# Kernel optimization log

Hardware: AMD Instinct MI355X
Metric: run time of the kernel (lower is better)

Reference implementation:

```python
import jax, jax.numpy as jnp
import numpy as np

ROPE_BASE = 10000.0
CHUNK = 2048
NEG_INF = -1e30


def _rope(q, k, start_index):
    # q, k: (B, T, H, Dh) with Dh even; half-split RoPE as in RotaryEmbedding
    B, T, H, Dh = q.shape
    half = Dh // 2
    inv_freq = jnp.exp(jnp.arange(half, dtype=jnp.float32) * (-(np.log(ROPE_BASE) / half)))
    pos = jnp.arange(T, dtype=jnp.float32) + jnp.float32(start_index)
    ang = pos[:, None] * inv_freq[None, :]              # (T, half)
    cos = jnp.cos(ang)[None, :, None, :].astype(q.dtype)  # (1,T,1,half)
    sin = jnp.sin(ang)[None, :, None, :].astype(q.dtype)

    def rot(x):
        x1, x2 = x[..., :half], x[..., half:]
        return jnp.concatenate([x1 * cos - x2 * sin, x2 * cos + x1 * sin], axis=-1)

    return rot(q), rot(k)


def reference(q, k, v, start_index):
    # Chunked causal self-attention, softmax(QK^T) V with scale = 1.0 (Megalodon Eq. 9).
    B, T, H, Dh = q.shape
    Dv = v.shape[-1]
    q, k = _rope(q, k, start_index)

    nc = T // CHUNK  # T assumed multiple of chunk_size (prefill path, no cache)
    qc = q.reshape(B, nc, CHUNK, H, Dh)
    kc = k.reshape(B, nc, CHUNK, H, Dh)
    vc = v.reshape(B, nc, CHUNK, H, Dv)

    # per-chunk causal mask (C, C): 0 where j <= i else -inf
    i = jnp.arange(CHUNK)
    causal = (i[None, :] <= i[:, None])

    scores = jnp.einsum('bnqhd,bnkhd->bnhqk', qc, kc)  # scale = 1.0
    scores = jnp.where(causal[None, None, None, :, :], scores, NEG_INF)
    probs = jax.nn.softmax(scores, axis=-1)
    out = jnp.einsum('bnhqk,bnkhd->bnqhd', probs, vc)
    return out.reshape(B, T, H, Dv)


def setup_inputs() -> dict:
    key = jax.random.key(0)
    kq, kk, kv = jax.random.split(key, 3)
    B, T, H, Dh, Dv = 2, 4096, 16, 128, 128
    return {
        'q': jax.random.normal(kq, (B, T, H, Dh), dtype=jnp.float32),
        'k': jax.random.normal(kk, (B, T, H, Dh), dtype=jnp.float32),
        'v': jax.random.normal(kv, (B, T, H, Dv), dtype=jnp.float32),
        'start_index': 0,
    }
```

## Files before the change

### kernel.cpp

```cpp
#include <hip/hip_runtime.h>


#define T_TOT  4096
#define HH     16
#define DH     128
#define CHUNKL 2048
#define QT     128
#define KTILE  64
#define THREADS 256
#define NEGV   1e30f
#define L2E    1.44269504088896f
#define THRL2  11.5415603f

typedef _Float16 f16;
typedef __attribute__((ext_vector_type(8)))  _Float16 f16x8;
typedef __attribute__((ext_vector_type(4)))  _Float16 f16x4;
typedef __attribute__((ext_vector_type(2)))  _Float16 f16x2;
typedef __attribute__((ext_vector_type(4)))  float    f32x4;
typedef __attribute__((ext_vector_type(16))) float    f32x16;
typedef __attribute__((ext_vector_type(4)))  int      i32x4;

#define AS_G(p) ((const __attribute__((address_space(1))) void*)(p))
#define AS_L(p) ((__attribute__((address_space(3))) void*)(p))

__device__ __forceinline__ f32x16 mfma32(f16x8 a, f16x8 b, f32x16 c) {
    return __builtin_amdgcn_mfma_f32_32x32x16_f16(a, b, c, 0, 0, 0);
}
__device__ __forceinline__ f32x4 mfma16(f16x8 a, f16x8 b, f32x4 c) {
    return __builtin_amdgcn_mfma_f32_16x16x32_f16(a, b, c, 0, 0, 0);
}
__device__ __forceinline__ int pk2(float a, float b) {
    f16x2 t; t[0] = (f16)a; t[1] = (f16)b;
    return __builtin_bit_cast(int, t);
}

__global__ void rope_table_kernel(float* __restrict__ tab, const int* __restrict__ startp) {
    int gid = blockIdx.x * blockDim.x + threadIdx.x;
    int t = gid >> 6, d = gid & 63;
    float pos  = (float)(t + *startp);
    float invf = expf((float)d * (-9.210340371976184f / 64.0f));
    float s, c;
    sincosf(pos * invf, &s, &c);
    tab[gid] = c;
    tab[T_TOT * 64 + gid] = s;
}

__global__ void prep_kv_kernel(const float* __restrict__ K, const float* __restrict__ V,
                               const float* __restrict__ tab,
                               f16* __restrict__ Kws, f16* __restrict__ VTws) {
    const int half = (2 * T_TOT * HH * DH) / 8;
    int gid = blockIdx.x * blockDim.x + threadIdx.x;
    if (gid < half) {
        const int tile = gid >> 10, idx = gid & 1023;
        const int key = idx >> 4, c8 = idx & 15;
        const int dsw0 = c8 << 3;
        const int sw   = (key & 7) << 3;
        const int d0   = dsw0 ^ sw;
        const int kt = tile & 31, h = (tile >> 5) & 15, n = (tile >> 9) & 1, b = tile >> 10;
        const int t  = n * CHUNKL + kt * KTILE + key;
        const float* kp = K + ((size_t)(b * T_TOT + t) * HH + h) * DH;
        const int dl = d0 & 63;
        f32x4 xm0 = *(const f32x4*)(kp + d0);
        f32x4 xm1 = *(const f32x4*)(kp + d0 + 4);
        f32x4 xo0 = *(const f32x4*)(kp + (d0 ^ 64));
        f32x4 xo1 = *(const f32x4*)(kp + (d0 ^ 64) + 4);
        f32x4 cc0 = *(const f32x4*)(tab + t * 64 + dl);
        f32x4 cc1 = *(const f32x4*)(tab + t * 64 + dl + 4);
        f32x4 ss0 = *(const f32x4*)(tab + T_TOT * 64 + t * 64 + dl);
        f32x4 ss1 = *(const f32x4*)(tab + T_TOT * 64 + t * 64 + dl + 4);
        const float sgn = (d0 < 64) ? -1.f : 1.f;
        f16x8 out;
#pragma unroll
        for (int j = 0; j < 4; ++j) {
            out[j]     = (f16)(xm0[j] * cc0[j] + sgn * xo0[j] * ss0[j]);
            out[4 + j] = (f16)(xm1[j] * cc1[j] + sgn * xo1[j] * ss1[j]);
        }
        *(f16x8*)&Kws[(size_t)tile * 8192 + key * DH + dsw0] = out;
    } else {
        const int oc = gid - half;
        const int tile = oc >> 10, idx = oc & 1023;
        const int d = idx >> 3, c8 = idx & 7;
        const int ksw0 = c8 << 3;
        const int sw   = (d & 7) << 3;
        const int key0 = ksw0 ^ sw;
        const int kt = tile & 31, h = (tile >> 5) & 15, n = (tile >> 9) & 1, b = tile >> 10;
        const int t0 = n * CHUNKL + kt * KTILE + key0;
        const float* vp = V + ((size_t)(b * T_TOT + t0) * HH + h) * DH + d;
        f16x8 out;
#pragma unroll
        for (int j = 0; j < 8; ++j)
            out[j] = (f16)vp[(size_t)j * (HH * DH)];
        *(f16x8*)&VTws[(size_t)tile * 8192 + d * KTILE + ksw0] = out;
    }
}

__global__ __launch_bounds__(THREADS, 2)
void attn_fast_kernel(const float* __restrict__ Q, const f16* __restrict__ Kws,
                      const f16* __restrict__ VTws, const float* __restrict__ tab,
                      float* __restrict__ O)
{
    __shared__ f16 Kl[2][KTILE * DH];
    __shared__ f16 VTl[2][KTILE * DH];

    const int bid = blockIdx.x;
    const int sb  = (bid & 7) * 128 + (bid >> 3);
    const int qt  = 15 - (sb & 15);
    const int bnh = sb >> 4;
    const int hd = bnh & 15, n = (bnh >> 4) & 1, b = bnh >> 5;

    const int tid = threadIdx.x;
    const int w   = tid >> 6;
    const int l   = tid & 63;
    const int hl  = l >> 5;
    const int c31 = l & 31;

    const int q0 = qt * QT;
    const size_t bh = (size_t)b * T_TOT * (HH * DH) + (size_t)hd * DH;
    const size_t tile0 = ((size_t)(((b * 2 + n) * 16 + hd) * 32)) * 8192;

    const int qr = q0 + w * 32 + c31;
    const int tg = n * CHUNKL + qr;
    const float* qp = Q + bh + (size_t)tg * (HH * DH);

    f16x8 qf[8];
#pragma unroll
    for (int ks = 0; ks < 8; ++ks) {
        const int dbase = ks * 16 + 8 * hl;
        const int dl    = dbase & 63;
        f32x4 xa0 = *(const f32x4*)(qp + dbase);
        f32x4 xa1 = *(const f32x4*)(qp + dbase + 4);
        f32x4 xb0 = *(const f32x4*)(qp + (dbase ^ 64));
        f32x4 xb1 = *(const f32x4*)(qp + (dbase ^ 64) + 4);
        float cc[8], ss[8];
        *(f32x4*)&cc[0] = *(const f32x4*)(tab + tg * 64 + dl);
        *(f32x4*)&cc[4] = *(const f32x4*)(tab + tg * 64 + dl + 4);
        *(f32x4*)&ss[0] = *(const f32x4*)(tab + T_TOT * 64 + tg * 64 + dl);
        *(f32x4*)&ss[4] = *(const f32x4*)(tab + T_TOT * 64 + tg * 64 + dl + 4);
        const float sgn = (dbase < 64) ? -1.f : 1.f;
        float xa[8] = {xa0[0],xa0[1],xa0[2],xa0[3],xa1[0],xa1[1],xa1[2],xa1[3]};
        float xb[8] = {xb0[0],xb0[1],xb0[2],xb0[3],xb1[0],xb1[1],xb1[2],xb1[3]};
        f16x8 f;
#pragma unroll
        for (int j = 0; j < 8; ++j)
            f[j] = (f16)((xa[j] * cc[j] + sgn * xb[j] * ss[j]) * L2E);
        qf[ks] = f;
    }

    f32x16 o[4];
    float mrun = -NEGV, lrun = 0.f;
#pragma unroll
    for (int dt = 0; dt < 4; ++dt)
#pragma unroll
        for (int r = 0; r < 16; ++r) o[dt][r] = 0.f;

    const int nkt = 2 * qt + 2;
    int cur = 0;

#pragma unroll
    for (int i = 0; i < 4; ++i) {
        const int off = (i * 4 + w) * 512;
        __builtin_amdgcn_global_load_lds(AS_G(Kws  + tile0 + off + l * 8), AS_L(&Kl[0][off]),  16, 0, 0);
        __builtin_amdgcn_global_load_lds(AS_G(VTws + tile0 + off + l * 8), AS_L(&VTl[0][off]), 16, 0, 0);
    }

    for (int kt = 0; kt < nkt; ++kt) {
        __syncthreads();

        if (kt + 1 < nkt) {
            const f16* ks_ = Kws  + tile0 + (size_t)(kt + 1) * 8192;
            const f16* vs_ = VTws + tile0 + (size_t)(kt + 1) * 8192;
            const int nb = cur ^ 1;
#pragma unroll
            for (int i = 0; i < 4; ++i) {
                const int off = (i * 4 + w) * 512;
                __builtin_amdgcn_global_load_lds(AS_G(ks_ + off + l * 8), AS_L(&Kl[nb][off]),  16, 0, 0);
                __builtin_amdgcn_global_load_lds(AS_G(vs_ + off + l * 8), AS_L(&VTl[nb][off]), 16, 0, 0);
            }
        }

        const bool active = (kt * KTILE) < (q0 + w * 32 + 32);
        if (active) {
            const f16* Klc  = Kl[cur];
            const f16* VTlc = VTl[cur];

            f32x16 s[2];
#pragma unroll
            for (int ts = 0; ts < 2; ++ts)
#pragma unroll
                for (int r = 0; r < 16; ++r) s[ts][r] = 0.f;

            __builtin_amdgcn_s_setprio(1);
#pragma unroll
            for (int ts = 0; ts < 2; ++ts) {
                const int key = ts * 32 + c31;
                const int swk = (key & 7) << 3;
#pragma unroll
                for (int ks = 0; ks < 8; ++ks) {
                    f16x8 kf = *(const f16x8*)&Klc[key * DH + ((ks * 16 + 8 * hl) ^ swk)];
                    s[ts] = mfma32(kf, qf[ks], s[ts]);
                }
            }
            __builtin_amdgcn_s_setprio(0);

            if (kt >= 2 * qt) {
#pragma unroll
                for (int ts = 0; ts < 2; ++ts)
#pragma unroll
                    for (int r = 0; r < 16; ++r) {
                        const int key = kt * KTILE + ts * 32 + (r & 3) + 8 * (r >> 2) + 4 * hl;
                        if (key > qr) s[ts][r] = -NEGV;
                    }
            }

            float mx = s[0][0];
#pragma unroll
            for (int r = 1; r < 16; ++r) mx = fmaxf(mx, s[0][r]);
#pragma unroll
            for (int r = 0; r < 16; ++r) mx = fmaxf(mx, s[1][r]);
            mx = fmaxf(mx, __shfl_xor(mx, 32));

            if (__any(mx > mrun + THRL2)) {
                const float mn = fmaxf(mrun, mx);
                const float al = exp2f(mrun - mn);
                mrun = mn;
                lrun *= al;
#pragma unroll
                for (int dt = 0; dt < 4; ++dt)
#pragma unroll
                    for (int r = 0; r < 16; ++r) o[dt][r] *= al;
            }

            float ps = 0.f;
#pragma unroll
            for (int ts = 0; ts < 2; ++ts)
#pragma unroll
                for (int r = 0; r < 16; ++r) {
                    const float p = exp2f(s[ts][r] - mrun);
                    s[ts][r] = p;
                    ps += p;
                }
            lrun += ps;

            f16x8 pb[4];
#pragma unroll
            for (int ts = 0; ts < 2; ++ts) {
#pragma unroll
                for (int gs = 0; gs < 2; ++gs) {
                    const int G = 8 * gs;
                    const int A  = pk2(s[ts][G + 0], s[ts][G + 1]);
                    const int Bw = pk2(s[ts][G + 2], s[ts][G + 3]);
                    const int C  = pk2(s[ts][G + 4], s[ts][G + 5]);
                    const int Dw = pk2(s[ts][G + 6], s[ts][G + 7]);
                    const int Y1 = hl ? A : C;
                    const int Y2 = hl ? Bw : Dw;
                    const int r1 = __shfl_xor(Y1, 32);
                    const int r2 = __shfl_xor(Y2, 32);
                    i32x4 bi;
                    bi[0] = hl ? r1 : A;
                    bi[1] = hl ? r2 : Bw;
                    bi[2] = hl ? C  : r1;
                    bi[3] = hl ? Dw : r2;
                    pb[2 * ts + gs] = __builtin_bit_cast(f16x8, bi);
                }
            }

            __builtin_amdgcn_s_setprio(1);
#pragma unroll
            for (int dt = 0; dt < 4; ++dt) {
                const int d   = dt * 32 + c31;
                const int swv = (d & 7) << 3;
#pragma unroll
                for (int ks = 0; ks < 4; ++ks) {
                    f16x8 vf = *(const f16x8*)&VTlc[d * KTILE + ((ks * 16 + 8 * hl) ^ swv)];
                    o[dt] = mfma32(vf, pb[ks], o[dt]);
                }
            }
            __builtin_amdgcn_s_setprio(0);
        }
        cur ^= 1;
    }

    const float lt  = lrun + __shfl_xor(lrun, 32);
    const float inv = 1.0f / lt;
    float* op = O + bh + (size_t)tg * (HH * DH);
#pragma unroll
    for (int dt = 0; dt < 4; ++dt) {
#pragma unroll
        for (int dd = 0; dd < 4; ++dd) {
            f32x4 val;
#pragma unroll
            for (int c = 0; c < 4; ++c) val[c] = o[dt][4 * dd + c] * inv;
            *(f32x4*)&op[dt * 32 + dd * 8 + 4 * hl] = val;
        }
    }
}

__global__ __launch_bounds__(THREADS, 2)
void attn_kernel(const float* __restrict__ Q, const float* __restrict__ K,
                 const float* __restrict__ V, const int* __restrict__ startp,
                 float* __restrict__ O)
{
    __shared__ f16 Kl[KTILE * DH];
    __shared__ f16 VTl[DH * KTILE];
    __shared__ f16 Pl[4][32 * 72];

    const int bid = blockIdx.x;
    const int qt  = 15 - (bid & 15);
    const int bnh = bid >> 4;
    const int h = bnh & 15, n = (bnh >> 4) & 1, b = bnh >> 5;

    const int tid  = threadIdx.x;
    const int w    = tid >> 6;
    const int lane = tid & 63;
    const int g    = lane >> 4, m = lane & 15;

    const int q0 = qt * QT;
    const size_t bh = (size_t)b * T_TOT * (HH * DH) + (size_t)h * DH;
    const int start = *startp;

    f16x8  qf[2][4];
    float  mrun[2][4], lrun[2][4];
    f32x4  o[2][8];
    const f32x4 ZERO4 = {0.f, 0.f, 0.f, 0.f};

#pragma unroll
    for (int rs = 0; rs < 2; ++rs) {
#pragma unroll
        for (int r = 0; r < 4; ++r) { mrun[rs][r] = -NEGV; lrun[rs][r] = 0.f; }
#pragma unroll
        for (int dt = 0; dt < 8; ++dt) o[rs][dt] = ZERO4;

        const int tg = n * CHUNKL + q0 + w * 32 + rs * 16 + m;
        const float* qp = Q + bh + (size_t)tg * (HH * DH);
#pragma unroll
        for (int kc = 0; kc < 4; ++kc) {
            const int dbase = kc * 32 + g * 8;
            const int dlo   = dbase & 63;
            f32x4 xa0 = *(const f32x4*)(qp + dbase);
            f32x4 xa1 = *(const f32x4*)(qp + dbase + 4);
            f32x4 xb0 = *(const f32x4*)(qp + (dbase ^ 64));
            f32x4 xb1 = *(const f32x4*)(qp + (dbase ^ 64) + 4);
            float cc[8], ss[8];
#pragma unroll
            for (int j = 0; j < 8; ++j) {
                float invf = expf((float)(dlo + j) * (-9.210340371976184f / 64.0f));
                sincosf((float)(tg + start) * invf, &ss[j], &cc[j]);
            }
            const float sgn = (dbase < 64) ? -1.f : 1.f;
            float xa[8] = {xa0[0],xa0[1],xa0[2],xa0[3],xa1[0],xa1[1],xa1[2],xa1[3]};
            float xb[8] = {xb0[0],xb0[1],xb0[2],xb0[3],xb1[0],xb1[1],xb1[2],xb1[3]};
            f16x8 f;
#pragma unroll
            for (int j = 0; j < 8; ++j) f[j] = (f16)(xa[j] * cc[j] + sgn * xb[j] * ss[j]);
            qf[rs][kc] = f;
        }
    }

    const int nkt = 2 * qt + 2;
    for (int kt = 0; kt < nkt; ++kt) {
        __syncthreads();
#pragma unroll
        for (int it = 0; it < 4; ++it) {
            const int tau = tid + THREADS * it;
            const int row = tau >> 4;
            const int d0  = (tau & 15) << 2;
            const int tg  = n * CHUNKL + kt * KTILE + row;
            const float* kp = K + bh + (size_t)tg * (HH * DH);
            f32x4 xa = *(const f32x4*)(kp + d0);
            f32x4 xb = *(const f32x4*)(kp + d0 + 64);
            f32x4 cc, ss;
#pragma unroll
            for (int j = 0; j < 4; ++j) {
                float invf = expf((float)(d0 + j) * (-9.210340371976184f / 64.0f));
                float sv, cv;
                sincosf((float)(tg + start) * invf, &sv, &cv);
                cc[j] = cv; ss[j] = sv;
            }
            f16x4 oA, oB;
#pragma unroll
            for (int j = 0; j < 4; ++j) {
                oA[j] = (f16)(xa[j] * cc[j] - xb[j] * ss[j]);
                oB[j] = (f16)(xb[j] * cc[j] + xa[j] * ss[j]);
            }
            const int sw = (row & 7) << 3;
            *(f16x4*)&Kl[row * DH + (d0 ^ sw)]        = oA;
            *(f16x4*)&Kl[row * DH + ((d0 + 64) ^ sw)] = oB;
        }
#pragma unroll
        for (int it = 0; it < 8; ++it) {
            const int tau = tid + THREADS * it;
            const int key = tau & 63;
            const int d0  = (tau >> 6) << 2;
            const int tg  = n * CHUNKL + kt * KTILE + key;
            f32x4 x = *(const f32x4*)(V + bh + (size_t)tg * (HH * DH) + d0);
#pragma unroll
            for (int j = 0; j < 4; ++j) {
                const int d = d0 + j;
                VTl[d * KTILE + (key ^ ((d & 7) << 3))] = (f16)x[j];
            }
        }
        __syncthreads();

        const bool active = (kt * KTILE) < (q0 + w * 32 + 32);
        if (active) {
            f32x4 sa[2][4];
#pragma unroll
            for (int rs = 0; rs < 2; ++rs)
#pragma unroll
                for (int nt = 0; nt < 4; ++nt) sa[rs][nt] = ZERO4;
#pragma unroll
            for (int nt = 0; nt < 4; ++nt) {
                const int key = nt * 16 + m;
                const int swk = (key & 7) << 3;
#pragma unroll
                for (int kc = 0; kc < 4; ++kc) {
                    f16x8 bf = *(const f16x8*)&Kl[key * DH + ((kc * 32 + g * 8) ^ swk)];
                    sa[0][nt] = mfma16(qf[0][kc], bf, sa[0][nt]);
                    sa[1][nt] = mfma16(qf[1][kc], bf, sa[1][nt]);
                }
            }
            const bool domask = (kt >= 2 * qt);
#pragma unroll
            for (int rs = 0; rs < 2; ++rs) {
                if (domask) {
#pragma unroll
                    for (int nt = 0; nt < 4; ++nt) {
                        const int key = kt * KTILE + nt * 16 + m;
#pragma unroll
                        for (int r = 0; r < 4; ++r) {
                            const int qr = q0 + w * 32 + rs * 16 + 4 * g + r;
                            if (key > qr) sa[rs][nt][r] = -NEGV;
                        }
                    }
                }
                float mx[4];
#pragma unroll
                for (int r = 0; r < 4; ++r)
                    mx[r] = fmaxf(fmaxf(sa[rs][0][r], sa[rs][1][r]),
                                  fmaxf(sa[rs][2][r], sa[rs][3][r]));
#pragma unroll
                for (int off = 1; off < 16; off <<= 1)
#pragma unroll
                    for (int r = 0; r < 4; ++r)
                        mx[r] = fmaxf(mx[r], __shfl_xor(mx[r], off));
                float al[4], ps[4];
#pragma unroll
                for (int r = 0; r < 4; ++r) {
                    const float mn = fmaxf(mrun[rs][r], mx[r]);
                    al[r] = exp2f((mrun[rs][r] - mn) * L2E);
                    mrun[rs][r] = mn;
                    ps[r] = 0.f;
                }
#pragma unroll
                for (int nt = 0; nt < 4; ++nt)
#pragma unroll
                    for (int r = 0; r < 4; ++r) {
                        const float p = exp2f((sa[rs][nt][r] - mrun[rs][r]) * L2E);
                        sa[rs][nt][r] = p;
                        ps[r] += p;
                    }
#pragma unroll
                for (int off = 1; off < 16; off <<= 1)
#pragma unroll
                    for (int r = 0; r < 4; ++r)
                        ps[r] += __shfl_xor(ps[r], off);
#pragma unroll
                for (int r = 0; r < 4; ++r)
                    lrun[rs][r] = lrun[rs][r] * al[r] + ps[r];
#pragma unroll
                for (int dt = 0; dt < 8; ++dt)
#pragma unroll
                    for (int r = 0; r < 4; ++r)
                        o[rs][dt][r] *= al[r];
#pragma unroll
                for (int nt = 0; nt < 4; ++nt)
#pragma unroll
                    for (int r = 0; r < 4; ++r)
                        Pl[w][(rs * 16 + 4 * g + r) * 72 + nt * 16 + m] = (f16)sa[rs][nt][r];
            }
            f16x8 pa[2][2];
#pragma unroll
            for (int rs = 0; rs < 2; ++rs)
#pragma unroll
                for (int kc = 0; kc < 2; ++kc)
                    pa[rs][kc] = *(const f16x8*)&Pl[w][(rs * 16 + m) * 72 + kc * 32 + g * 8];
#pragma unroll
            for (int dt = 0; dt < 8; ++dt) {
                const int d   = dt * 16 + m;
                const int swv = (d & 7) << 3;
#pragma unroll
                for (int kc = 0; kc < 2; ++kc) {
                    f16x8 vf = *(const f16x8*)&VTl[d * KTILE + ((kc * 32 + g * 8) ^ swv)];
                    o[0][dt] = mfma16(pa[0][kc], vf, o[0][dt]);
                    o[1][dt] = mfma16(pa[1][kc], vf, o[1][dt]);
                }
            }
        }
    }

#pragma unroll
    for (int rs = 0; rs < 2; ++rs) {
#pragma unroll
        for (int r = 0; r < 4; ++r) {
            const float inv = 1.0f / lrun[rs][r];
            const int tg = n * CHUNKL + q0 + w * 32 + rs * 16 + 4 * g + r;
            float* op = O + bh + (size_t)tg * (HH * DH);
#pragma unroll
            for (int dt = 0; dt < 8; ++dt)
                op[dt * 16 + m] = o[rs][dt][r] * inv;
        }
    }
}

extern "C" void kernel_launch(void* const* d_in, const int* in_sizes, int n_in,
                              void* d_out, int out_size, void* d_ws, size_t ws_size,
                              hipStream_t stream) {
    const float* q = (const float*)d_in[0];
    const float* k = (const float*)d_in[1];
    const float* v = (const float*)d_in[2];
    const int* start = (const int*)d_in[3];
    float* out = (float*)d_out;

    const size_t tab_elems = (size_t)2 * T_TOT * 64;
    const size_t kv_elems  = (size_t)2 * T_TOT * HH * DH;
    const size_t need = tab_elems * sizeof(float) + 2 * kv_elems * sizeof(f16);
    const int nblocks = 64 * 16;

    if (ws_size >= need) {
        float* tab = (float*)d_ws;
        f16* Kws  = (f16*)((char*)d_ws + tab_elems * sizeof(float));
        f16* VTws = Kws + kv_elems;
        rope_table_kernel<<<(T_TOT * 64) / THREADS, THREADS, 0, stream>>>(tab, start);
        prep_kv_kernel<<<(int)(2 * (kv_elems / 8) / THREADS), THREADS, 0, stream>>>(k, v, tab, Kws, VTws);
        attn_fast_kernel<<<nblocks, THREADS, 0, stream>>>(q, Kws, VTws, tab, out);
    } else {
        attn_kernel<<<nblocks, THREADS, 0, stream>>>(q, k, v, start, out);
    }
}
```

Measured before the change: 234.6 us.

## Pair complementary query tiles per 512-thread block to balance causal work

Each attention block now has 8 waves and handles two query tiles, pr and 15-pr, so every block carries roughly equal causal work and the grid shrinks to 512 blocks. The K/V tiles staged in LDS are shared by both query tiles, which halves global-to-LDS traffic per query. Waves on the shorter tile go idle on later iterations but still take part in the barriers. Launch bounds change to 512 threads with 4 blocks per SM, which may tighten the register budget and cause spills.

```diff
diff --git a/kernel.cpp b/kernel.cpp
--- a/kernel.cpp
+++ b/kernel.cpp
@@ -7,7 +7,6 @@
 #define CHUNKL 2048
 #define QT     128
 #define KTILE  64
-#define THREADS 256
 #define NEGV   1e30f
 #define L2E    1.44269504088896f
 #define THRL2  11.5415603f
@@ -94,7 +93,7 @@
     }
 }
 
-__global__ __launch_bounds__(THREADS, 2)
+__global__ __launch_bounds__(512, 4)
 void attn_fast_kernel(const float* __restrict__ Q, const f16* __restrict__ Kws,
                       const f16* __restrict__ VTws, const float* __restrict__ tab,
                       float* __restrict__ O)
@@ -103,22 +102,25 @@
     __shared__ f16 VTl[2][KTILE * DH];
 
     const int bid = blockIdx.x;
-    const int sb  = (bid & 7) * 128 + (bid >> 3);
-    const int qt  = 15 - (sb & 15);
-    const int bnh = sb >> 4;
+    const int sb  = (bid & 7) * 64 + (bid >> 3);
+    const int pr  = sb & 7;
+    const int bnh = sb >> 3;
     const int hd = bnh & 15, n = (bnh >> 4) & 1, b = bnh >> 5;
+    const int qtA = pr, qtB = 15 - pr;
 
     const int tid = threadIdx.x;
     const int w   = tid >> 6;
+    const int wq  = w & 3;
     const int l   = tid & 63;
     const int hl  = l >> 5;
     const int c31 = l & 31;
 
-    const int q0 = qt * QT;
+    const int qt_w = (w < 4) ? qtA : qtB;
+    const int q0   = qt_w * QT;
     const size_t bh = (size_t)b * T_TOT * (HH * DH) + (size_t)hd * DH;
     const size_t tile0 = ((size_t)(((b * 2 + n) * 16 + hd) * 32)) * 8192;
 
-    const int qr = q0 + w * 32 + c31;
+    const int qr = q0 + wq * 32 + c31;
     const int tg = n * CHUNKL + qr;
     const float* qp = Q + bh + (size_t)tg * (HH * DH);
 
@@ -153,12 +155,12 @@
 #pragma unroll
         for (int r = 0; r < 16; ++r) o[dt][r] = 0.f;
 
-    const int nkt = 2 * qt + 2;
+    const int nkt = 2 * qtB + 2;
     int cur = 0;
 
 #pragma unroll
-    for (int i = 0; i < 4; ++i) {
-        const int off = (i * 4 + w) * 512;
+    for (int i = 0; i < 2; ++i) {
+        const int off = (i * 8 + w) * 512;
         __builtin_amdgcn_global_load_lds(AS_G(Kws  + tile0 + off + l * 8), AS_L(&Kl[0][off]),  16, 0, 0);
         __builtin_amdgcn_global_load_lds(AS_G(VTws + tile0 + off + l * 8), AS_L(&VTl[0][off]), 16, 0, 0);
     }
@@ -171,14 +173,14 @@
             const f16* vs_ = VTws + tile0 + (size_t)(kt + 1) * 8192;
             const int nb = cur ^ 1;
 #pragma unroll
-            for (int i = 0; i < 4; ++i) {
-                const int off = (i * 4 + w) * 512;
+            for (int i = 0; i < 2; ++i) {
+                const int off = (i * 8 + w) * 512;
                 __builtin_amdgcn_global_load_lds(AS_G(ks_ + off + l * 8), AS_L(&Kl[nb][off]),  16, 0, 0);
                 __builtin_amdgcn_global_load_lds(AS_G(vs_ + off + l * 8), AS_L(&VTl[nb][off]), 16, 0, 0);
             }
         }
 
-        const bool active = (kt * KTILE) < (q0 + w * 32 + 32);
+        const bool active = (kt * KTILE) < (q0 + wq * 32 + 32);
         if (active) {
             const f16* Klc  = Kl[cur];
             const f16* VTlc = VTl[cur];
@@ -202,7 +204,7 @@
             }
             __builtin_amdgcn_s_setprio(0);
 
-            if (kt >= 2 * qt) {
+            if (kt >= 2 * qt_w) {
 #pragma unroll
                 for (int ts = 0; ts < 2; ++ts)
 #pragma unroll
@@ -295,7 +297,7 @@
     }
 }
 
-__global__ __launch_bounds__(THREADS, 2)
+__global__ __launch_bounds__(256, 2)
 void attn_kernel(const float* __restrict__ Q, const float* __restrict__ K,
                  const float* __restrict__ V, const int* __restrict__ startp,
                  float* __restrict__ O)
@@ -361,7 +363,7 @@
         __syncthreads();
 #pragma unroll
         for (int it = 0; it < 4; ++it) {
-            const int tau = tid + THREADS * it;
+            const int tau = tid + 256 * it;
             const int row = tau >> 4;
             const int d0  = (tau & 15) << 2;
             const int tg  = n * CHUNKL + kt * KTILE + row;
@@ -388,7 +390,7 @@
         }
 #pragma unroll
         for (int it = 0; it < 8; ++it) {
-            const int tau = tid + THREADS * it;
+            const int tau = tid + 256 * it;
             const int key = tau & 63;
             const int d0  = (tau >> 6) << 2;
             const int tg  = n * CHUNKL + kt * KTILE + key;
@@ -524,16 +526,15 @@
     const size_t tab_elems = (size_t)2 * T_TOT * 64;
     const size_t kv_elems  = (size_t)2 * T_TOT * HH * DH;
     const size_t need = tab_elems * sizeof(float) + 2 * kv_elems * sizeof(f16);
-    const int nblocks = 64 * 16;
 
     if (ws_size >= need) {
         float* tab = (float*)d_ws;
         f16* Kws  = (f16*)((char*)d_ws + tab_elems * sizeof(float));
         f16* VTws = Kws + kv_elems;
-        rope_table_kernel<<<(T_TOT * 64) / THREADS, THREADS, 0, stream>>>(tab, start);
-        prep_kv_kernel<<<(int)(2 * (kv_elems / 8) / THREADS), THREADS, 0, stream>>>(k, v, tab, Kws, VTws);
-        attn_fast_kernel<<<nblocks, THREADS, 0, stream>>>(q, Kws, VTws, tab, out);
+        rope_table_kernel<<<(T_TOT * 64) / 256, 256, 0, stream>>>(tab, start);
+        prep_kv_kernel<<<(int)(2 * (kv_elems / 8) / 256), 256, 0, stream>>>(k, v, tab, Kws, VTws);
+        attn_fast_kernel<<<512, 512, 0, stream>>>(q, Kws, VTws, tab, out);
     } else {
-        attn_kernel<<<nblocks, THREADS, 0, stream>>>(q, k, v, start, out);
-    }
-}
+        attn_kernel<<<64 * 16, 256, 0, stream>>>(q, k, v, start, out);
+    }
+}
```

Measured after the change: 451.9 us. 92.6% more time.
